# Kernel optimization log

Measured on AMD Instinct MI355X. Metric: run time of the kernel, lower is better.

Reference implementation:

```python
import jax, jax.numpy as jnp
import numpy as np

MARGIN = 1.0   # TripletLoss(margin) init arg
EPS = 1e-6     # torch F.pairwise_distance eps used by nn.TripletMarginLoss
INF = 1e9

N, D_EMB, N_CLASSES = 8192, 1024, 128


def setup_inputs() -> dict:
    key = jax.random.key(0)
    k1, k2 = jax.random.split(key)
    embeddings = jax.random.normal(k1, (N, D_EMB), dtype=jnp.float32)
    target = jax.random.randint(k2, (N,), 0, N_CLASSES, dtype=jnp.int64 if jax.config.jax_enable_x64 else jnp.int32)
    return {"embeddings": embeddings, "target": target}


def _mine_and_loss(embeddings, target):
    # Vectorized, deterministic equivalent of the per-anchor random mining loop:
    # full pairwise L2 distance matrix via a GEMM (compute-bound core).
    sq = jnp.sum(embeddings * embeddings, axis=1)                      # [N]
    d2 = sq[:, None] + sq[None, :] - 2.0 * (embeddings @ embeddings.T)  # [N, N]
    Dm = jnp.sqrt(jnp.maximum(d2, 0.0))                                 # [N, N]

    same = target[:, None] == target[None, :]
    eye = jnp.eye(target.shape[0], dtype=bool)
    pos_mask = same & ~eye          # valid positives (same class, not self)
    neg_mask = ~same                # valid negatives (different class)

    # Positive: hardest (farthest) same-class sample (deterministic stand-in
    # for the original's random positive draw).
    pos_scores = jnp.where(pos_mask, Dm, -INF)
    pos_idx = jnp.argmax(pos_scores, axis=1)                           # [N]
    d_p = jnp.max(pos_scores, axis=1)                                  # [N]

    # Negative: semi-hard (d_p < d_n < d_p + margin), pick the closest such
    # negative; if none exists, fall back to the overall hardest (min-dist)
    # negative -- mirrors the loop's early-break vs. min_dist fallback.
    semi = neg_mask & (Dm > d_p[:, None]) & (Dm < (d_p + MARGIN)[:, None])
    has_semi = jnp.any(semi, axis=1)
    neg_semi = jnp.argmin(jnp.where(semi, Dm, INF), axis=1)
    neg_hard = jnp.argmin(jnp.where(neg_mask, Dm, INF), axis=1)
    neg_idx = jnp.where(has_semi, neg_semi, neg_hard)                  # [N]

    # nn.TripletMarginLoss(margin, p=2): mean(relu(d(a,p) - d(a,n) + margin))
    # with torch's pairwise_distance eps added to the difference.
    a = embeddings
    p = embeddings[pos_idx]
    n = embeddings[neg_idx]
    dp = jnp.sqrt(jnp.sum((a - p + EPS) ** 2, axis=1))
    dn = jnp.sqrt(jnp.sum((a - n + EPS) ** 2, axis=1))
    return jnp.mean(jax.nn.relu(dp - dn + MARGIN))


def reference(embeddings, target):
    return _mine_and_loss(embeddings, target)
```

## Files before the change

### kernel.cpp

```cpp
#include <hip/hip_runtime.h>
#include <hip/hip_bf16.h>

#define N 8192
#define D 1024
#define MARGIN 1.0f
#define EPS 1e-6f

typedef __attribute__((ext_vector_type(8))) short bf16x8;
typedef __attribute__((ext_vector_type(4))) float f32x4;
typedef __attribute__((ext_vector_type(8))) _Float16 f16x8;
typedef __attribute__((ext_vector_type(4))) _Float16 f16x4;
typedef __attribute__((ext_vector_type(8))) unsigned short u16x8;

__device__ inline unsigned short f2bf(float x) {
    unsigned u = __float_as_uint(x);
    unsigned r = (u + 0x7FFFu + ((u >> 16) & 1u)) >> 16;
    return (unsigned short)r;
}

__device__ inline float h2f(unsigned hb) {
    return (float)__builtin_bit_cast(_Float16, (unsigned short)hb);
}

__global__ __launch_bounds__(256) void prep_kernel(const float* __restrict__ E,
                                                   const int* __restrict__ target,
                                                   unsigned short* __restrict__ Ebf,
                                                   float* __restrict__ sq,
                                                   unsigned char* __restrict__ cls) {
    const int r = blockIdx.x;
    const int tid = threadIdx.x;
    const float4 v = ((const float4*)(E + (size_t)r * D))[tid];
    ushort4 o;
    o.x = f2bf(v.x); o.y = f2bf(v.y); o.z = f2bf(v.z); o.w = f2bf(v.w);
    ((ushort4*)(Ebf + (size_t)r * D))[tid] = o;
    float s = v.x * v.x + v.y * v.y + v.z * v.z + v.w * v.w;
    for (int off = 32; off > 0; off >>= 1) s += __shfl_down(s, off);
    __shared__ float red[4];
    const int lane = tid & 63, wave = tid >> 6;
    if (lane == 0) red[wave] = s;
    __syncthreads();
    if (tid == 0) {
        sq[r] = red[0] + red[1] + red[2] + red[3];
        cls[r] = (unsigned char)target[r];
    }
}


#define SLOT_0A0 0
#define SLOT_0A1 16384
#define SLOT_0B0 32768
#define SLOT_0B1 49152
#define SLOT_1A0 65536
#define SLOT_1A1 81920
#define SLOT_1B0 98304
#define SLOT_1B1 114688

#define VMW(n) __asm__ __volatile__("s_waitcnt vmcnt(" #n ")" ::: "memory")
#define NOSTAGE ((void)0)
#define NOWAIT ((void)0)

#define STAGE(slotOff, baseRow, kcol) do {                                              \
    const unsigned short* _s0 = E + (size_t)((baseRow) + (tid >> 2)) * D + (kcol) + stc * 8; \
    __builtin_amdgcn_global_load_lds(                                                    \
        (const __attribute__((address_space(1))) unsigned int*)_s0,                      \
        (__attribute__((address_space(3))) unsigned int*)(smem + (slotOff) + wave * 1024), 16, 0, 0); \
    const unsigned short* _s1 = _s0 + (size_t)128 * D;                                   \
    __builtin_amdgcn_global_load_lds(                                                    \
        (const __attribute__((address_space(1))) unsigned int*)_s1,                      \
        (__attribute__((address_space(3))) unsigned int*)(smem + (slotOff) + 8192 + wave * 1024), 16, 0, 0); \
} while (0)

#define PHASE(b, ks, mq, LOADB, STG, WAIT) do {                                          \
    const char* _As = smem + (b) * 65536 + (ks) * 16384;                                 \
    const char* _Bs = smem + (b) * 65536 + 32768 + (ks) * 16384;                         \
    if (LOADB) {                                                                         \
        _Pragma("unroll") for (int nj = 0; nj < 4; ++nj)                                 \
            bfr[nj] = *(const bf16x8*)(_Bs + (wn * 64 + nj * 16 + mr) * 64 + swz);       \
    }                                                                                    \
    bf16x8 af[4];                                                                        \
    _Pragma("unroll") for (int mi = 0; mi < 4; ++mi)                                     \
        af[mi] = *(const bf16x8*)(_As + (wm * 128 + (mq) * 64 + mi * 16 + mr) * 64 + swz); \
    STG;                                                                                 \
    __builtin_amdgcn_s_setprio(1);                                                       \
    _Pragma("unroll") for (int mi = 0; mi < 4; ++mi)                                     \
        _Pragma("unroll") for (int nj = 0; nj < 4; ++nj)                                 \
            acc[(mq) * 4 + mi][nj] = __builtin_amdgcn_mfma_f32_16x16x32_bf16(            \
                af[mi], bfr[nj], acc[(mq) * 4 + mi][nj], 0, 0, 0);                       \
    __builtin_amdgcn_s_setprio(0);                                                       \
    WAIT;                                                                                \
    __asm__ __volatile__("s_barrier" ::: "memory");                                      \
} while (0)

__device__ __forceinline__ void diag_path(char* smem,
                                          const unsigned short* __restrict__ E,
                                          const float* __restrict__ sq,
                                          _Float16* __restrict__ D2h,
                                          const int c, const int tid) {
    const int lane = tid & 63;
    const int wave = tid >> 6;
    const int wmL = wave >> 2;
    const int wnL = wave & 3;
    const int mr = lane & 15;
    const int q = lane >> 4;
    const int kq = q * 8;

    const int t = c / 3, s = c - 3 * t;
    const int smi = (s + 1) >> 1;
    const int sni = s >> 1;
    const int rm = t * 256 + smi * 128;
    const int cn = t * 256 + sni * 128;
    const bool offdiag = (s == 1);

    f32x4 acc[4][2] = {};

#define DSTAGE(sl, kk) do {                                                              \
    __builtin_amdgcn_global_load_lds(                                                    \
        (const __attribute__((address_space(1))) unsigned int*)(E + (size_t)(rm + (tid >> 2)) * D + (kk) * 32 + (tid & 3) * 8), \
        (__attribute__((address_space(3))) unsigned int*)(smem + (sl) * 32768 + wave * 1024), 16, 0, 0); \
    __builtin_amdgcn_global_load_lds(                                                    \
        (const __attribute__((address_space(1))) unsigned int*)(E + (size_t)(cn + (tid >> 2)) * D + (kk) * 32 + (tid & 3) * 8), \
        (__attribute__((address_space(3))) unsigned int*)(smem + (sl) * 32768 + 16384 + wave * 1024), 16, 0, 0); \
} while (0)

#define DCOMPUTE(k) do {                                                                 \
    const unsigned short* As = (const unsigned short*)(smem + (size_t)((k) & 3) * 32768);\
    const unsigned short* Bs = As + 8192;                                                \
    bf16x8 af[4], bfv[2];                                                                \
    _Pragma("unroll") for (int mi = 0; mi < 4; ++mi)                                     \
        af[mi] = *(const bf16x8*)(As + (wmL * 64 + mi * 16 + mr) * 32 + kq);             \
    _Pragma("unroll") for (int ni = 0; ni < 2; ++ni)                                     \
        bfv[ni] = *(const bf16x8*)(Bs + (wnL * 32 + ni * 16 + mr) * 32 + kq);            \
    _Pragma("unroll") for (int mi = 0; mi < 4; ++mi)                                     \
        _Pragma("unroll") for (int ni = 0; ni < 2; ++ni)                                 \
            acc[mi][ni] = __builtin_amdgcn_mfma_f32_16x16x32_bf16(af[mi], bfv[ni], acc[mi][ni], 0, 0, 0); \
} while (0)

    DSTAGE(0, 0);
    DSTAGE(1, 1);
    for (int k = 0; k < 30; ++k) {
        DSTAGE((k + 2) & 3, k + 2);
        __asm__ __volatile__("s_waitcnt vmcnt(4)" ::: "memory");
        __asm__ __volatile__("s_barrier" ::: "memory");
        DCOMPUTE(k);
    }
    __asm__ __volatile__("s_waitcnt vmcnt(2)" ::: "memory");
    __asm__ __volatile__("s_barrier" ::: "memory");
    DCOMPUTE(30);
    __asm__ __volatile__("s_waitcnt vmcnt(0)" ::: "memory");
    __asm__ __volatile__("s_barrier" ::: "memory");
    DCOMPUTE(31);
#undef DSTAGE
#undef DCOMPUTE
    __syncthreads();

    _Float16* Ts = (_Float16*)smem;
    float sqjL[2];
#pragma unroll
    for (int ni = 0; ni < 2; ++ni) sqjL[ni] = sq[cn + wnL * 32 + ni * 16 + mr];
#pragma unroll
    for (int mi = 0; mi < 4; ++mi) {
        const int lrow = wmL * 64 + mi * 16 + q * 4;
        const int i0 = rm + lrow;
        const f32x4 sqi = *(const f32x4*)(sq + i0);
#pragma unroll
        for (int ni = 0; ni < 2; ++ni) {
            const int lcol = wnL * 32 + ni * 16 + mr;
            const int j = cn + lcol;
            f16x4 tv;
#pragma unroll
            for (int r = 0; r < 4; ++r) {
                const float d2 = fmaxf(sqi[r] + sqjL[ni] - 2.0f * acc[mi][ni][r], 0.0f);
                const _Float16 h = (_Float16)d2;
                D2h[(size_t)(i0 + r) * N + j] = h;
                tv[r] = h;
            }
            if (offdiag)
                *(f16x4*)(Ts + (size_t)lcol * 136 + lrow) = tv;
        }
    }
    if (offdiag) {
        __syncthreads();
#pragma unroll
        for (int it = 0; it < 4; ++it) {
            const int rt = it * 32 + (tid >> 4);
            const int seg = tid & 15;
            f16x8 v = *(const f16x8*)(Ts + (size_t)rt * 136 + seg * 8);
            *(f16x8*)(D2h + (size_t)(cn + rt) * N + rm + seg * 8) = v;
        }
    }
}

__global__ __launch_bounds__(512, 2) void gemm_kernel(const unsigned short* __restrict__ E,
                                                      const float* __restrict__ sq,
                                                      _Float16* __restrict__ D2h) {
    extern __shared__ char smem[];

    const int tid = threadIdx.x;

    if (blockIdx.x >= 496) {
        diag_path(smem, E, sq, D2h, blockIdx.x - 496, tid);
        return;
    }

    const int lane = tid & 63;
    const int wave = tid >> 6;
    const int wm = wave >> 2;
    const int wn = wave & 3;
    const int mr = lane & 15;
    const int q = lane >> 4;
    const int swz = ((q ^ ((mr >> 1) & 3)) << 4);
    const int stc = (tid & 3) ^ ((tid >> 3) & 3);

    const int h = blockIdx.x;
    const int l = (h & 7) * 62 + (h >> 3);

    int by = (int)((1.0f + sqrtf(8.0f * (float)l + 1.0f)) * 0.5f);
    while (by * (by - 1) / 2 > l) --by;
    while ((by + 1) * by / 2 <= l) ++by;
    const int bx = l - by * (by - 1) / 2;
    const int rm = by * 256;
    const int cn = bx * 256;

    f32x4 acc[8][4] = {};
    bf16x8 bfr[4];

    STAGE(SLOT_0A0, rm, 0);
    STAGE(SLOT_0B0, cn, 0);
    STAGE(SLOT_0A1, rm, 32);
    STAGE(SLOT_0B1, cn, 32);
    STAGE(SLOT_1A0, rm, 64);
    VMW(6);
    __asm__ __volatile__("s_barrier" ::: "memory");

    for (int i = 0; i < 7; ++i) {
        const int kt = 2 * i;
        PHASE(0, 0, 0, 1, STAGE(SLOT_1B0, cn, (kt + 1) * 64 + 0),  NOWAIT);
        PHASE(0, 0, 1, 0, STAGE(SLOT_1A1, rm, (kt + 1) * 64 + 32), VMW(6));
        PHASE(0, 1, 0, 1, STAGE(SLOT_1B1, cn, (kt + 1) * 64 + 32), NOWAIT);
        PHASE(0, 1, 1, 0, STAGE(SLOT_0A0, rm, (kt + 2) * 64 + 0),  VMW(6));
        PHASE(1, 0, 0, 1, STAGE(SLOT_0B0, cn, (kt + 2) * 64 + 0),  NOWAIT);
        PHASE(1, 0, 1, 0, STAGE(SLOT_0A1, rm, (kt + 2) * 64 + 32), VMW(6));
        PHASE(1, 1, 0, 1, STAGE(SLOT_0B1, cn, (kt + 2) * 64 + 32), NOWAIT);
        PHASE(1, 1, 1, 0, STAGE(SLOT_1A0, rm, (kt + 3) * 64 + 0),  VMW(6));
    }
    PHASE(0, 0, 0, 1, STAGE(SLOT_1B0, cn, 15 * 64 + 0),  NOWAIT);
    PHASE(0, 0, 1, 0, STAGE(SLOT_1A1, rm, 15 * 64 + 32), VMW(6));
    PHASE(0, 1, 0, 1, STAGE(SLOT_1B1, cn, 15 * 64 + 32), NOWAIT);
    PHASE(0, 1, 1, 0, NOSTAGE, VMW(4));
    PHASE(1, 0, 0, 1, NOSTAGE, NOWAIT);
    PHASE(1, 0, 1, 0, NOSTAGE, VMW(0));
    PHASE(1, 1, 0, 1, NOSTAGE, NOWAIT);
    PHASE(1, 1, 1, 0, NOSTAGE, NOWAIT);

    __asm__ __volatile__("s_waitcnt lgkmcnt(0)" ::: "memory");
    __asm__ __volatile__("s_barrier" ::: "memory");

    const int crow = q * 4;
    float sqj[4];
#pragma unroll
    for (int nj = 0; nj < 4; ++nj) sqj[nj] = sq[cn + wn * 64 + nj * 16 + mr];
    float sqiv[8][4];
#pragma unroll
    for (int mg = 0; mg < 8; ++mg) {
        const f32x4 s4 = *(const f32x4*)(sq + rm + wm * 128 + mg * 16 + crow);
#pragma unroll
        for (int r = 0; r < 4; ++r) sqiv[mg][r] = s4[r];
    }

#pragma unroll
    for (int mg = 0; mg < 8; ++mg) {
        const int ilocb = wm * 128 + mg * 16 + crow;
#pragma unroll
        for (int nj = 0; nj < 4; ++nj) {
            const int jloc = wn * 64 + nj * 16 + mr;
            const unsigned jc = (unsigned)jloc >> 3;
            const unsigned jo = ((unsigned)jloc & 7) << 1;
#pragma unroll
            for (int r = 0; r < 4; ++r) {
                const float d2 = fmaxf(sqiv[mg][r] + sqj[nj] - 2.0f * acc[mg][nj][r], 0.0f);
                const int row = ilocb + r;
                *(_Float16*)(smem + (size_t)row * 512 + ((jc ^ (row & 31)) << 4) + jo) = (_Float16)d2;
            }
        }
    }
    __asm__ __volatile__("s_waitcnt lgkmcnt(0)" ::: "memory");
    __asm__ __volatile__("s_barrier" ::: "memory");
    {
        const int seg = tid & 31;
#pragma unroll
        for (int it = 0; it < 16; ++it) {
            const int rt = it * 16 + (tid >> 5);
            f16x8 v = *(const f16x8*)(smem + (size_t)rt * 512 + (((unsigned)seg ^ (rt & 31)) << 4));
            *(f16x8*)(D2h + (size_t)(rm + rt) * N + cn + seg * 8) = v;
        }
    }
    __asm__ __volatile__("s_waitcnt lgkmcnt(0)" ::: "memory");
    __asm__ __volatile__("s_barrier" ::: "memory");

#pragma unroll
    for (int mg = 0; mg < 8; ++mg) {
        const int iloc = wm * 128 + mg * 16 + crow;
        const unsigned cch = (unsigned)iloc >> 3;
        const unsigned cof = ((unsigned)iloc & 7) << 1;
#pragma unroll
        for (int nj = 0; nj < 4; ++nj) {
            const int jloc = wn * 64 + nj * 16 + mr;
            f16x4 tv;
#pragma unroll
            for (int r = 0; r < 4; ++r)
                tv[r] = (_Float16)fmaxf(sqiv[mg][r] + sqj[nj] - 2.0f * acc[mg][nj][r], 0.0f);
            *(f16x4*)(smem + (size_t)jloc * 512 + ((cch ^ (jloc & 31)) << 4) + cof) = tv;
        }
    }
    __asm__ __volatile__("s_waitcnt lgkmcnt(0)" ::: "memory");
    __asm__ __volatile__("s_barrier" ::: "memory");
    {
        const int seg = tid & 31;
#pragma unroll
        for (int it = 0; it < 16; ++it) {
            const int rt = it * 16 + (tid >> 5);
            f16x8 v = *(const f16x8*)(smem + (size_t)rt * 512 + (((unsigned)seg ^ (rt & 31)) << 4));
            *(f16x8*)(D2h + (size_t)(cn + rt) * N + rm + seg * 8) = v;
        }
    }
}

__global__ __launch_bounds__(256) void mine_kernel(const _Float16* __restrict__ D2h,
                                                   const unsigned char* __restrict__ cls,
                                                   float* __restrict__ loss_arr) {
    const int i = blockIdx.x;
    const int tid = threadIdx.x;
    const int lane = tid & 63, wave = tid >> 6;
    const unsigned tcb = cls[i];
    const unsigned short* row = (const unsigned short*)(D2h + (size_t)i * N);

    u16x8 v[4];
    unsigned long long c8[4];
#pragma unroll
    for (int it = 0; it < 4; ++it) {
        v[it] = *(const u16x8*)(row + it * 2048 + tid * 8);
        c8[it] = *(const unsigned long long*)(cls + it * 2048 + tid * 8);
    }

    unsigned pm = 0u, nm = 0xFFFFu;
#pragma unroll
    for (int it = 0; it < 4; ++it) {
#pragma unroll
        for (int e = 0; e < 8; ++e) {
            const unsigned hb = v[it][e];
            const bool s = ((unsigned)(c8[it] >> (8 * e)) & 0xFFu) == tcb;
            pm = max(pm, s ? hb : 0u);
            nm = min(nm, s ? 0xFFFFu : hb);
        }
    }
    for (int off = 1; off < 64; off <<= 1) {
        pm = max(pm, (unsigned)__shfl_xor((int)pm, off));
        nm = min(nm, (unsigned)__shfl_xor((int)nm, off));
    }
    __shared__ unsigned redp[4], redn[4], reds[4];
    if (lane == 0) { redp[wave] = pm; redn[wave] = nm; }
    __syncthreads();
    pm = max(max(redp[0], redp[1]), max(redp[2], redp[3]));
    nm = min(min(redn[0], redn[1]), min(redn[2], redn[3]));
    const unsigned lob = pm;

    unsigned sm = 0xFFFFu;
#pragma unroll
    for (int it = 0; it < 4; ++it) {
#pragma unroll
        for (int e = 0; e < 8; ++e) {
            const unsigned hb = v[it][e];
            sm = min(sm, hb > lob ? hb : 0xFFFFu);
        }
    }
    for (int off = 1; off < 64; off <<= 1)
        sm = min(sm, (unsigned)__shfl_xor((int)sm, off));
    if (lane == 0) reds[wave] = sm;
    __syncthreads();
    if (tid == 0) {
        sm = min(min(reds[0], reds[1]), min(reds[2], reds[3]));
        const float lo = h2f(lob);
        const float dp = sqrtf(lo);
        const float hw = dp + MARGIN;
        const float hi = hw * hw;
        const float smv = h2f(sm);
        const float dn2 = (smv < hi) ? smv : h2f(nm);
        loss_arr[i] = fmaxf(dp - sqrtf(dn2) + MARGIN, 0.0f);
    }
}

__global__ __launch_bounds__(256) void reduce_kernel(const float* __restrict__ loss_arr,
                                                     float* __restrict__ out) {
    const int tid = threadIdx.x;
    float s = 0.0f;
    for (int k = tid; k < N; k += 256) s += loss_arr[k];
    for (int off = 32; off > 0; off >>= 1) s += __shfl_down(s, off);
    __shared__ float red[4];
    const int lane = tid & 63, wave = tid >> 6;
    if (lane == 0) red[wave] = s;
    __syncthreads();
    if (tid == 0) out[0] = (red[0] + red[1] + red[2] + red[3]) * (1.0f / N);
}

extern "C" void kernel_launch(void* const* d_in, const int* in_sizes, int n_in,
                              void* d_out, int out_size, void* d_ws, size_t ws_size,
                              hipStream_t stream) {
    const float* E = (const float*)d_in[0];
    const int* target = (const int*)d_in[1];
    float* out = (float*)d_out;
    char* ws = (char*)d_ws;

    unsigned short* Ebf = (unsigned short*)ws;
    float* sq        = (float*)(ws + (size_t)16777216);
    float* loss_arr  = (float*)(ws + (size_t)16809984);
    unsigned char* cls = (unsigned char*)(ws + (size_t)16842752);
    _Float16* D2h    = (_Float16*)(ws + (size_t)16875520);

    static bool attr_set = false;
    if (!attr_set) {
        hipFuncSetAttribute((const void*)gemm_kernel,
                            hipFuncAttributeMaxDynamicSharedMemorySize, 131072);
        attr_set = true;
    }

    prep_kernel<<<N, 256, 0, stream>>>(E, target, Ebf, sq, cls);
    gemm_kernel<<<592, 512, 131072, stream>>>(Ebf, sq, D2h);
    mine_kernel<<<N, 256, 0, stream>>>(D2h, cls, loss_arr);
    reduce_kernel<<<1, 256, 0, stream>>>(loss_arr, out);
}
```

Before: 192.7 us.

## Batch rows per block in prep and mine kernels; reorder GEMM tile mapping

The prep kernel now handles four rows per block, one wave per row, which drops the shared-memory reduction and barrier. The mine kernel processes two distance rows per block so the class-label loads are shared between them and the launch count is halved. The GEMM triangular tile index mapping is replaced with a grouped scheme that walks 4-row strips, changing which tiles run concurrently and so their L2 reuse. The risks are more register pressure in the mine kernel and a new tile mapping that must still cover every lower-triangular tile exactly once.

New measurement: 185.8 us. -3.6%, faster.

```diff
diff --git a/kernel.cpp b/kernel.cpp
--- a/kernel.cpp
+++ b/kernel.cpp
@@ -27,20 +27,17 @@
                                                    unsigned short* __restrict__ Ebf,
                                                    float* __restrict__ sq,
                                                    unsigned char* __restrict__ cls) {
-    const int r = blockIdx.x;
     const int tid = threadIdx.x;
-    const float4 v = ((const float4*)(E + (size_t)r * D))[tid];
+    const int lane = tid & 63, wave = tid >> 6;
+    const int r = blockIdx.x * 4 + wave;
+    const float4 v = ((const float4*)(E + (size_t)r * D))[lane];
     ushort4 o;
     o.x = f2bf(v.x); o.y = f2bf(v.y); o.z = f2bf(v.z); o.w = f2bf(v.w);
-    ((ushort4*)(Ebf + (size_t)r * D))[tid] = o;
+    ((ushort4*)(Ebf + (size_t)r * D))[lane] = o;
     float s = v.x * v.x + v.y * v.y + v.z * v.z + v.w * v.w;
     for (int off = 32; off > 0; off >>= 1) s += __shfl_down(s, off);
-    __shared__ float red[4];
-    const int lane = tid & 63, wave = tid >> 6;
-    if (lane == 0) red[wave] = s;
-    __syncthreads();
-    if (tid == 0) {
-        sq[r] = red[0] + red[1] + red[2] + red[3];
+    if (lane == 0) {
+        sq[r] = s;
         cls[r] = (unsigned char)target[r];
     }
 }
@@ -214,10 +211,20 @@
     const int h = blockIdx.x;
     const int l = (h & 7) * 62 + (h >> 3);
 
-    int by = (int)((1.0f + sqrtf(8.0f * (float)l + 1.0f)) * 0.5f);
-    while (by * (by - 1) / 2 > l) --by;
-    while ((by + 1) * by / 2 <= l) ++by;
-    const int bx = l - by * (by - 1) / 2;
+    int s = (int)((2.0f + sqrtf(4.0f + 32.0f * (float)l)) * 0.0625f);
+    while (8 * (s + 1) * (s + 1) - 2 * (s + 1) <= l) ++s;
+    while (8 * s * s - 2 * s > l) --s;
+    const int o = l - (8 * s * s - 2 * s);
+    int by, bx;
+    if (o < 16 * s) {
+        bx = o >> 2;
+        by = 4 * s + (o & 3);
+    } else {
+        const int o2 = o - 16 * s;
+        if (o2 < 3)      { bx = 4 * s;     by = 4 * s + 1 + o2; }
+        else if (o2 < 5) { bx = 4 * s + 1; by = 4 * s + 2 + (o2 - 3); }
+        else             { bx = 4 * s + 2; by = 4 * s + 3; }
+    }
     const int rm = by * 256;
     const int cn = bx * 256;
 
@@ -328,64 +335,88 @@
 __global__ __launch_bounds__(256) void mine_kernel(const _Float16* __restrict__ D2h,
                                                    const unsigned char* __restrict__ cls,
                                                    float* __restrict__ loss_arr) {
-    const int i = blockIdx.x;
+    const int i0 = blockIdx.x * 2;
     const int tid = threadIdx.x;
     const int lane = tid & 63, wave = tid >> 6;
-    const unsigned tcb = cls[i];
-    const unsigned short* row = (const unsigned short*)(D2h + (size_t)i * N);
-
-    u16x8 v[4];
+    const unsigned tcbA = cls[i0];
+    const unsigned tcbB = cls[i0 + 1];
+    const unsigned short* rowA = (const unsigned short*)(D2h + (size_t)i0 * N);
+    const unsigned short* rowB = rowA + N;
+
+    u16x8 va[4], vb[4];
     unsigned long long c8[4];
 #pragma unroll
     for (int it = 0; it < 4; ++it) {
-        v[it] = *(const u16x8*)(row + it * 2048 + tid * 8);
+        va[it] = *(const u16x8*)(rowA + it * 2048 + tid * 8);
+        vb[it] = *(const u16x8*)(rowB + it * 2048 + tid * 8);
         c8[it] = *(const unsigned long long*)(cls + it * 2048 + tid * 8);
     }
 
-    unsigned pm = 0u, nm = 0xFFFFu;
+    unsigned pmA = 0u, nmA = 0xFFFFu, pmB = 0u, nmB = 0xFFFFu;
 #pragma unroll
     for (int it = 0; it < 4; ++it) {
 #pragma unroll
         for (int e = 0; e < 8; ++e) {
-            const unsigned hb = v[it][e];
-            const bool s = ((unsigned)(c8[it] >> (8 * e)) & 0xFFu) == tcb;
-            pm = max(pm, s ? hb : 0u);
-            nm = min(nm, s ? 0xFFFFu : hb);
+            const unsigned cv = (unsigned)(c8[it] >> (8 * e)) & 0xFFu;
+            const unsigned ha = va[it][e];
+            const unsigned hb = vb[it][e];
+            const bool sA = (cv == tcbA);
+            const bool sB = (cv == tcbB);
+            pmA = max(pmA, sA ? ha : 0u);
+            nmA = min(nmA, sA ? 0xFFFFu : ha);
+            pmB = max(pmB, sB ? hb : 0u);
+            nmB = min(nmB, sB ? 0xFFFFu : hb);
         }
     }
     for (int off = 1; off < 64; off <<= 1) {
-        pm = max(pm, (unsigned)__shfl_xor((int)pm, off));
-        nm = min(nm, (unsigned)__shfl_xor((int)nm, off));
-    }
-    __shared__ unsigned redp[4], redn[4], reds[4];
-    if (lane == 0) { redp[wave] = pm; redn[wave] = nm; }
+        pmA = max(pmA, (unsigned)__shfl_xor((int)pmA, off));
+        nmA = min(nmA, (unsigned)__shfl_xor((int)nmA, off));
+        pmB = max(pmB, (unsigned)__shfl_xor((int)pmB, off));
+        nmB = min(nmB, (unsigned)__shfl_xor((int)nmB, off));
+    }
+    __shared__ unsigned redp[2][4], redn[2][4], reds[2][4];
+    if (lane == 0) {
+        redp[0][wave] = pmA; redn[0][wave] = nmA;
+        redp[1][wave] = pmB; redn[1][wave] = nmB;
+    }
     __syncthreads();
-    pm = max(max(redp[0], redp[1]), max(redp[2], redp[3]));
-    nm = min(min(redn[0], redn[1]), min(redn[2], redn[3]));
-    const unsigned lob = pm;
-
-    unsigned sm = 0xFFFFu;
+    pmA = max(max(redp[0][0], redp[0][1]), max(redp[0][2], redp[0][3]));
+    nmA = min(min(redn[0][0], redn[0][1]), min(redn[0][2], redn[0][3]));
+    pmB = max(max(redp[1][0], redp[1][1]), max(redp[1][2], redp[1][3]));
+    nmB = min(min(redn[1][0], redn[1][1]), min(redn[1][2], redn[1][3]));
+
+    unsigned smA = 0xFFFFu, smB = 0xFFFFu;
 #pragma unroll
     for (int it = 0; it < 4; ++it) {
 #pragma unroll
         for (int e = 0; e < 8; ++e) {
-            const unsigned hb = v[it][e];
-            sm = min(sm, hb > lob ? hb : 0xFFFFu);
-        }
-    }
-    for (int off = 1; off < 64; off <<= 1)
-        sm = min(sm, (unsigned)__shfl_xor((int)sm, off));
-    if (lane == 0) reds[wave] = sm;
+            const unsigned ha = va[it][e];
+            const unsigned hb = vb[it][e];
+            smA = min(smA, ha > pmA ? ha : 0xFFFFu);
+            smB = min(smB, hb > pmB ? hb : 0xFFFFu);
+        }
+    }
+    for (int off = 1; off < 64; off <<= 1) {
+        smA = min(smA, (unsigned)__shfl_xor((int)smA, off));
+        smB = min(smB, (unsigned)__shfl_xor((int)smB, off));
+    }
+    if (lane == 0) { reds[0][wave] = smA; reds[1][wave] = smB; }
     __syncthreads();
     if (tid == 0) {
-        sm = min(min(reds[0], reds[1]), min(reds[2], reds[3]));
-        const float lo = h2f(lob);
-        const float dp = sqrtf(lo);
-        const float hw = dp + MARGIN;
-        const float hi = hw * hw;
-        const float smv = h2f(sm);
-        const float dn2 = (smv < hi) ? smv : h2f(nm);
-        loss_arr[i] = fmaxf(dp - sqrtf(dn2) + MARGIN, 0.0f);
+#pragma unroll
+        for (int rr = 0; rr < 2; ++rr) {
+            const unsigned lob = rr ? pmB : pmA;
+            const unsigned nm = rr ? nmB : nmA;
+            const unsigned sm = min(min(reds[rr][0], reds[rr][1]),
+                                    min(reds[rr][2], reds[rr][3]));
+            const float lo = h2f(lob);
+            const float dp = sqrtf(lo);
+            const float hw = dp + MARGIN;
+            const float hi = hw * hw;
+            const float smv = h2f(sm);
+            const float dn2 = (smv < hi) ? smv : h2f(nm);
+            loss_arr[i0 + rr] = fmaxf(dp - sqrtf(dn2) + MARGIN, 0.0f);
+        }
     }
 }
 
@@ -423,8 +454,8 @@
         attr_set = true;
     }
 
-    prep_kernel<<<N, 256, 0, stream>>>(E, target, Ebf, sq, cls);
+    prep_kernel<<<N / 4, 256, 0, stream>>>(E, target, Ebf, sq, cls);
     gemm_kernel<<<592, 512, 131072, stream>>>(Ebf, sq, D2h);
-    mine_kernel<<<N, 256, 0, stream>>>(D2h, cls, loss_arr);
+    mine_kernel<<<N / 2, 256, 0, stream>>>(D2h, cls, loss_arr);
     reduce_kernel<<<1, 256, 0, stream>>>(loss_arr, out);
 }
```

## Fuse positive/hardest-negative mining into GEMM epilogue, drop symmetric transpose write

Applied to the files above, without the earlier changes.

The GEMM epilogue now computes per-row and per-column hardest-positive and hardest-negative values directly from the accumulators. It reduces them through shared-memory atomics and then global atomicMax/atomicMin. Because the symmetric tile is covered by column reductions, the transposed half of the fp16 distance matrix is no longer written. The old full-row mine kernel is replaced by a tile-wise semi-hard pass over the upper triangle only, plus a small finalize kernel. This halves the distance-matrix traffic, at the cost of many atomics and an extra launch. The prep kernel is also repacked to one row per wave and now initialises the reduction buffers.

Measured after the change: 204.5 us. +6.2%, slower.

```diff
diff --git a/kernel.cpp b/kernel.cpp
--- a/kernel.cpp
+++ b/kernel.cpp
@@ -22,26 +22,33 @@
     return (float)__builtin_bit_cast(_Float16, (unsigned short)hb);
 }
 
+__device__ inline unsigned h2u(float d2) {
+    return (unsigned)__builtin_bit_cast(unsigned short, (_Float16)d2);
+}
+
 __global__ __launch_bounds__(256) void prep_kernel(const float* __restrict__ E,
                                                    const int* __restrict__ target,
                                                    unsigned short* __restrict__ Ebf,
                                                    float* __restrict__ sq,
-                                                   unsigned char* __restrict__ cls) {
-    const int r = blockIdx.x;
+                                                   unsigned char* __restrict__ cls,
+                                                   unsigned* __restrict__ pmG,
+                                                   unsigned* __restrict__ nmG,
+                                                   unsigned* __restrict__ smG) {
     const int tid = threadIdx.x;
-    const float4 v = ((const float4*)(E + (size_t)r * D))[tid];
+    const int lane = tid & 63, wave = tid >> 6;
+    const int r = blockIdx.x * 4 + wave;
+    const float4 v = ((const float4*)(E + (size_t)r * D))[lane];
     ushort4 o;
     o.x = f2bf(v.x); o.y = f2bf(v.y); o.z = f2bf(v.z); o.w = f2bf(v.w);
-    ((ushort4*)(Ebf + (size_t)r * D))[tid] = o;
+    ((ushort4*)(Ebf + (size_t)r * D))[lane] = o;
     float s = v.x * v.x + v.y * v.y + v.z * v.z + v.w * v.w;
     for (int off = 32; off > 0; off >>= 1) s += __shfl_down(s, off);
-    __shared__ float red[4];
-    const int lane = tid & 63, wave = tid >> 6;
-    if (lane == 0) red[wave] = s;
-    __syncthreads();
-    if (tid == 0) {
-        sq[r] = red[0] + red[1] + red[2] + red[3];
+    if (lane == 0) {
+        sq[r] = s;
         cls[r] = (unsigned char)target[r];
+        pmG[r] = 0u;
+        nmG[r] = 0xFFFFFFFFu;
+        smG[r] = 0xFFFFFFFFu;
     }
 }
 
@@ -94,7 +101,10 @@
 __device__ __forceinline__ void diag_path(char* smem,
                                           const unsigned short* __restrict__ E,
                                           const float* __restrict__ sq,
+                                          const unsigned char* __restrict__ cls,
                                           _Float16* __restrict__ D2h,
+                                          unsigned* __restrict__ pmG,
+                                          unsigned* __restrict__ nmG,
                                           const int c, const int tid) {
     const int lane = tid & 63;
     const int wave = tid >> 6;
@@ -109,7 +119,6 @@
     const int sni = s >> 1;
     const int rm = t * 256 + smi * 128;
     const int cn = t * 256 + sni * 128;
-    const bool offdiag = (s == 1);
 
     f32x4 acc[4][2] = {};
 
@@ -153,52 +162,108 @@
 #undef DCOMPUTE
     __syncthreads();
 
-    _Float16* Ts = (_Float16*)smem;
+    unsigned ccbL[2];
     float sqjL[2];
 #pragma unroll
-    for (int ni = 0; ni < 2; ++ni) sqjL[ni] = sq[cn + wnL * 32 + ni * 16 + mr];
+    for (int ni = 0; ni < 2; ++ni) {
+        const int col = cn + wnL * 32 + ni * 16 + mr;
+        sqjL[ni] = sq[col];
+        ccbL[ni] = cls[col];
+    }
+
 #pragma unroll
     for (int mi = 0; mi < 4; ++mi) {
-        const int lrow = wmL * 64 + mi * 16 + q * 4;
-        const int i0 = rm + lrow;
+        const int i0 = rm + wmL * 64 + mi * 16 + q * 4;
         const f32x4 sqi = *(const f32x4*)(sq + i0);
 #pragma unroll
         for (int ni = 0; ni < 2; ++ni) {
-            const int lcol = wnL * 32 + ni * 16 + mr;
-            const int j = cn + lcol;
-            f16x4 tv;
+            const int j = cn + wnL * 32 + ni * 16 + mr;
 #pragma unroll
             for (int r = 0; r < 4; ++r) {
                 const float d2 = fmaxf(sqi[r] + sqjL[ni] - 2.0f * acc[mi][ni][r], 0.0f);
-                const _Float16 h = (_Float16)d2;
-                D2h[(size_t)(i0 + r) * N + j] = h;
-                tv[r] = h;
-            }
-            if (offdiag)
-                *(f16x4*)(Ts + (size_t)lcol * 136 + lrow) = tv;
-        }
-    }
-    if (offdiag) {
-        __syncthreads();
-#pragma unroll
-        for (int it = 0; it < 4; ++it) {
-            const int rt = it * 32 + (tid >> 4);
-            const int seg = tid & 15;
-            f16x8 v = *(const f16x8*)(Ts + (size_t)rt * 136 + seg * 8);
-            *(f16x8*)(D2h + (size_t)(cn + rt) * N + rm + seg * 8) = v;
-        }
+                D2h[(size_t)(i0 + r) * N + j] = (_Float16)d2;
+            }
+        }
+    }
+
+    unsigned* pmRowL = (unsigned*)smem;
+    unsigned* nmRowL = pmRowL + 128;
+    unsigned* pmColL = pmRowL + 256;
+    unsigned* nmColL = pmRowL + 384;
+    if (tid < 128)       pmRowL[tid] = 0u;
+    else if (tid < 256)  nmRowL[tid - 128] = 0xFFFFFFFFu;
+    else if (tid < 384)  pmColL[tid - 256] = 0u;
+    else                 nmColL[tid - 384] = 0xFFFFFFFFu;
+    __syncthreads();
+
+    unsigned cpm[2] = {0u, 0u}, cnm[2] = {0xFFFFu, 0xFFFFu};
+#pragma unroll
+    for (int mi = 0; mi < 4; ++mi) {
+        const int i0 = rm + wmL * 64 + mi * 16 + q * 4;
+        const unsigned clsR = *(const unsigned*)(cls + i0);
+        const f32x4 sqi = *(const f32x4*)(sq + i0);
+        unsigned rpm[4] = {0u, 0u, 0u, 0u};
+        unsigned rnm[4] = {0xFFFFu, 0xFFFFu, 0xFFFFu, 0xFFFFu};
+#pragma unroll
+        for (int ni = 0; ni < 2; ++ni) {
+#pragma unroll
+            for (int r = 0; r < 4; ++r) {
+                const unsigned v = h2u(fmaxf(sqi[r] + sqjL[ni] - 2.0f * acc[mi][ni][r], 0.0f));
+                const bool same = ((clsR >> (8 * r)) & 0xFFu) == ccbL[ni];
+                rpm[r] = max(rpm[r], same ? v : 0u);
+                rnm[r] = min(rnm[r], same ? 0xFFFFu : v);
+                cpm[ni] = max(cpm[ni], same ? v : 0u);
+                cnm[ni] = min(cnm[ni], same ? 0xFFFFu : v);
+            }
+        }
+#pragma unroll
+        for (int r = 0; r < 4; ++r) {
+            for (int off = 1; off < 16; off <<= 1) {
+                rpm[r] = max(rpm[r], (unsigned)__shfl_xor((int)rpm[r], off));
+                rnm[r] = min(rnm[r], (unsigned)__shfl_xor((int)rnm[r], off));
+            }
+            if (mr == 0) {
+                const int li = wmL * 64 + mi * 16 + q * 4 + r;
+                atomicMax(&pmRowL[li], rpm[r]);
+                atomicMin(&nmRowL[li], rnm[r]);
+            }
+        }
+    }
+#pragma unroll
+    for (int ni = 0; ni < 2; ++ni) {
+        cpm[ni] = max(cpm[ni], (unsigned)__shfl_xor((int)cpm[ni], 16));
+        cpm[ni] = max(cpm[ni], (unsigned)__shfl_xor((int)cpm[ni], 32));
+        cnm[ni] = min(cnm[ni], (unsigned)__shfl_xor((int)cnm[ni], 16));
+        cnm[ni] = min(cnm[ni], (unsigned)__shfl_xor((int)cnm[ni], 32));
+        if (q == 0) {
+            const int lj = wnL * 32 + ni * 16 + mr;
+            atomicMax(&pmColL[lj], cpm[ni]);
+            atomicMin(&nmColL[lj], cnm[ni]);
+        }
+    }
+    __syncthreads();
+    if (tid < 128) {
+        atomicMax(&pmG[rm + tid], pmRowL[tid]);
+        atomicMin(&nmG[rm + tid], nmRowL[tid]);
+    } else if (tid < 256) {
+        const int c2 = tid - 128;
+        atomicMax(&pmG[cn + c2], pmColL[c2]);
+        atomicMin(&nmG[cn + c2], nmColL[c2]);
     }
 }
 
 __global__ __launch_bounds__(512, 2) void gemm_kernel(const unsigned short* __restrict__ E,
                                                       const float* __restrict__ sq,
-                                                      _Float16* __restrict__ D2h) {
+                                                      const unsigned char* __restrict__ cls,
+                                                      _Float16* __restrict__ D2h,
+                                                      unsigned* __restrict__ pmG,
+                                                      unsigned* __restrict__ nmG) {
     extern __shared__ char smem[];
 
     const int tid = threadIdx.x;
 
     if (blockIdx.x >= 496) {
-        diag_path(smem, E, sq, D2h, blockIdx.x - 496, tid);
+        diag_path(smem, E, sq, cls, D2h, pmG, nmG, blockIdx.x - 496, tid);
         return;
     }
 
@@ -213,7 +278,6 @@
 
     const int h = blockIdx.x;
     const int l = (h & 7) * 62 + (h >> 3);
-
     int by = (int)((1.0f + sqrtf(8.0f * (float)l + 1.0f)) * 0.5f);
     while (by * (by - 1) / 2 > l) --by;
     while ((by + 1) * by / 2 <= l) ++by;
@@ -257,8 +321,13 @@
 
     const int crow = q * 4;
     float sqj[4];
-#pragma unroll
-    for (int nj = 0; nj < 4; ++nj) sqj[nj] = sq[cn + wn * 64 + nj * 16 + mr];
+    unsigned ccb[4];
+#pragma unroll
+    for (int nj = 0; nj < 4; ++nj) {
+        const int col = cn + wn * 64 + nj * 16 + mr;
+        sqj[nj] = sq[col];
+        ccb[nj] = cls[col];
+    }
     float sqiv[8][4];
 #pragma unroll
     for (int mg = 0; mg < 8; ++mg) {
@@ -297,96 +366,185 @@
     __asm__ __volatile__("s_waitcnt lgkmcnt(0)" ::: "memory");
     __asm__ __volatile__("s_barrier" ::: "memory");
 
+    unsigned* pmRow = (unsigned*)smem;
+    unsigned* nmRow = pmRow + 256;
+    unsigned* pmCol = pmRow + 512;
+    unsigned* nmCol = pmRow + 768;
+    if (tid < 256) { pmRow[tid] = 0u; nmRow[tid] = 0xFFFFFFFFu; }
+    else           { pmCol[tid - 256] = 0u; nmCol[tid - 256] = 0xFFFFFFFFu; }
+    __syncthreads();
+
+    unsigned cpm[4] = {0u, 0u, 0u, 0u};
+    unsigned cnm[4] = {0xFFFFu, 0xFFFFu, 0xFFFFu, 0xFFFFu};
 #pragma unroll
     for (int mg = 0; mg < 8; ++mg) {
-        const int iloc = wm * 128 + mg * 16 + crow;
-        const unsigned cch = (unsigned)iloc >> 3;
-        const unsigned cof = ((unsigned)iloc & 7) << 1;
+        const unsigned clsR = *(const unsigned*)(cls + rm + wm * 128 + mg * 16 + crow);
+        unsigned rpm[4] = {0u, 0u, 0u, 0u};
+        unsigned rnm[4] = {0xFFFFu, 0xFFFFu, 0xFFFFu, 0xFFFFu};
 #pragma unroll
         for (int nj = 0; nj < 4; ++nj) {
-            const int jloc = wn * 64 + nj * 16 + mr;
-            f16x4 tv;
-#pragma unroll
-            for (int r = 0; r < 4; ++r)
-                tv[r] = (_Float16)fmaxf(sqiv[mg][r] + sqj[nj] - 2.0f * acc[mg][nj][r], 0.0f);
-            *(f16x4*)(smem + (size_t)jloc * 512 + ((cch ^ (jloc & 31)) << 4) + cof) = tv;
-        }
-    }
-    __asm__ __volatile__("s_waitcnt lgkmcnt(0)" ::: "memory");
-    __asm__ __volatile__("s_barrier" ::: "memory");
-    {
-        const int seg = tid & 31;
-#pragma unroll
-        for (int it = 0; it < 16; ++it) {
-            const int rt = it * 16 + (tid >> 5);
-            f16x8 v = *(const f16x8*)(smem + (size_t)rt * 512 + (((unsigned)seg ^ (rt & 31)) << 4));
-            *(f16x8*)(D2h + (size_t)(cn + rt) * N + rm + seg * 8) = v;
-        }
-    }
-}
-
-__global__ __launch_bounds__(256) void mine_kernel(const _Float16* __restrict__ D2h,
-                                                   const unsigned char* __restrict__ cls,
-                                                   float* __restrict__ loss_arr) {
-    const int i = blockIdx.x;
+#pragma unroll
+            for (int r = 0; r < 4; ++r) {
+                const unsigned v = h2u(fmaxf(sqiv[mg][r] + sqj[nj] - 2.0f * acc[mg][nj][r], 0.0f));
+                const bool same = ((clsR >> (8 * r)) & 0xFFu) == ccb[nj];
+                rpm[r] = max(rpm[r], same ? v : 0u);
+                rnm[r] = min(rnm[r], same ? 0xFFFFu : v);
+                cpm[nj] = max(cpm[nj], same ? v : 0u);
+                cnm[nj] = min(cnm[nj], same ? 0xFFFFu : v);
+            }
+        }
+#pragma unroll
+        for (int r = 0; r < 4; ++r) {
+            for (int off = 1; off < 16; off <<= 1) {
+                rpm[r] = max(rpm[r], (unsigned)__shfl_xor((int)rpm[r], off));
+                rnm[r] = min(rnm[r], (unsigned)__shfl_xor((int)rnm[r], off));
+            }
+            if (mr == 0) {
+                const int li = wm * 128 + mg * 16 + crow + r;
+                atomicMax(&pmRow[li], rpm[r]);
+                atomicMin(&nmRow[li], rnm[r]);
+            }
+        }
+    }
+#pragma unroll
+    for (int nj = 0; nj < 4; ++nj) {
+        cpm[nj] = max(cpm[nj], (unsigned)__shfl_xor((int)cpm[nj], 16));
+        cpm[nj] = max(cpm[nj], (unsigned)__shfl_xor((int)cpm[nj], 32));
+        cnm[nj] = min(cnm[nj], (unsigned)__shfl_xor((int)cnm[nj], 16));
+        cnm[nj] = min(cnm[nj], (unsigned)__shfl_xor((int)cnm[nj], 32));
+        if (q == 0) {
+            const int lj = wn * 64 + nj * 16 + mr;
+            atomicMax(&pmCol[lj], cpm[nj]);
+            atomicMin(&nmCol[lj], cnm[nj]);
+        }
+    }
+    __syncthreads();
+    if (tid < 256) {
+        atomicMax(&pmG[rm + tid], pmRow[tid]);
+        atomicMin(&nmG[rm + tid], nmRow[tid]);
+    } else {
+        const int c2 = tid - 256;
+        atomicMax(&pmG[cn + c2], pmCol[c2]);
+        atomicMin(&nmG[cn + c2], nmCol[c2]);
+    }
+}
+
+__global__ __launch_bounds__(512) void mine2_kernel(const _Float16* __restrict__ D2h,
+                                                    const unsigned* __restrict__ pmG,
+                                                    unsigned* __restrict__ smG) {
+    __shared__ unsigned colMin[256];
     const int tid = threadIdx.x;
-    const int lane = tid & 63, wave = tid >> 6;
-    const unsigned tcb = cls[i];
-    const unsigned short* row = (const unsigned short*)(D2h + (size_t)i * N);
-
-    u16x8 v[4];
-    unsigned long long c8[4];
-#pragma unroll
-    for (int it = 0; it < 4; ++it) {
-        v[it] = *(const u16x8*)(row + it * 2048 + tid * 8);
-        c8[it] = *(const unsigned long long*)(cls + it * 2048 + tid * 8);
-    }
-
-    unsigned pm = 0u, nm = 0xFFFFu;
-#pragma unroll
-    for (int it = 0; it < 4; ++it) {
-#pragma unroll
-        for (int e = 0; e < 8; ++e) {
-            const unsigned hb = v[it][e];
-            const bool s = ((unsigned)(c8[it] >> (8 * e)) & 0xFFu) == tcb;
-            pm = max(pm, s ? hb : 0u);
-            nm = min(nm, s ? 0xFFFFu : hb);
-        }
-    }
-    for (int off = 1; off < 64; off <<= 1) {
-        pm = max(pm, (unsigned)__shfl_xor((int)pm, off));
-        nm = min(nm, (unsigned)__shfl_xor((int)nm, off));
-    }
-    __shared__ unsigned redp[4], redn[4], reds[4];
-    if (lane == 0) { redp[wave] = pm; redn[wave] = nm; }
-    __syncthreads();
-    pm = max(max(redp[0], redp[1]), max(redp[2], redp[3]));
-    nm = min(min(redn[0], redn[1]), min(redn[2], redn[3]));
-    const unsigned lob = pm;
-
-    unsigned sm = 0xFFFFu;
-#pragma unroll
-    for (int it = 0; it < 4; ++it) {
-#pragma unroll
-        for (int e = 0; e < 8; ++e) {
-            const unsigned hb = v[it][e];
-            sm = min(sm, hb > lob ? hb : 0xFFFFu);
-        }
-    }
-    for (int off = 1; off < 64; off <<= 1)
-        sm = min(sm, (unsigned)__shfl_xor((int)sm, off));
-    if (lane == 0) reds[wave] = sm;
-    __syncthreads();
-    if (tid == 0) {
-        sm = min(min(reds[0], reds[1]), min(reds[2], reds[3]));
-        const float lo = h2f(lob);
-        const float dp = sqrtf(lo);
-        const float hw = dp + MARGIN;
-        const float hi = hw * hw;
-        const float smv = h2f(sm);
-        const float dn2 = (smv < hi) ? smv : h2f(nm);
-        loss_arr[i] = fmaxf(dp - sqrtf(dn2) + MARGIN, 0.0f);
-    }
+    const int lane = tid & 63;
+
+    if (blockIdx.x < 496) {
+        const int l = blockIdx.x;
+        int by = (int)((1.0f + sqrtf(8.0f * (float)l + 1.0f)) * 0.5f);
+        while (by * (by - 1) / 2 > l) --by;
+        while ((by + 1) * by / 2 <= l) ++by;
+        const int bx = l - by * (by - 1) / 2;
+        const int rm = by * 256;
+        const int cn = bx * 256;
+
+        const int tr = tid >> 4;
+        const int tc = tid & 15;
+        unsigned pmc[16], cmin[16];
+#pragma unroll
+        for (int k = 0; k < 16; ++k) { pmc[k] = pmG[cn + tc * 16 + k]; cmin[k] = 0xFFFFu; }
+#pragma unroll
+        for (int ri = 0; ri < 8; ++ri) {
+            const int r = tr + 32 * ri;
+            const unsigned short* rp = (const unsigned short*)(D2h + (size_t)(rm + r) * N + cn + tc * 16);
+            const u16x8 a = *(const u16x8*)rp;
+            const u16x8 b = *(const u16x8*)(rp + 8);
+            const unsigned pmr = pmG[rm + r];
+            unsigned rmin = 0xFFFFu;
+#pragma unroll
+            for (int k = 0; k < 8; ++k) {
+                const unsigned v = a[k];
+                rmin = min(rmin, v > pmr ? v : 0xFFFFu);
+                cmin[k] = min(cmin[k], v > pmc[k] ? v : 0xFFFFu);
+                const unsigned w = b[k];
+                rmin = min(rmin, w > pmr ? w : 0xFFFFu);
+                cmin[k + 8] = min(cmin[k + 8], w > pmc[k + 8] ? w : 0xFFFFu);
+            }
+            for (int off = 1; off < 16; off <<= 1)
+                rmin = min(rmin, (unsigned)__shfl_xor((int)rmin, off));
+            if (tc == 0) atomicMin(&smG[rm + r], rmin);
+        }
+#pragma unroll
+        for (int k = 0; k < 16; ++k) {
+            cmin[k] = min(cmin[k], (unsigned)__shfl_xor((int)cmin[k], 16));
+            cmin[k] = min(cmin[k], (unsigned)__shfl_xor((int)cmin[k], 32));
+        }
+        if (tid < 256) colMin[tid] = 0xFFFFu;
+        __syncthreads();
+        if (lane < 16) {
+#pragma unroll
+            for (int k = 0; k < 16; ++k) atomicMin(&colMin[tc * 16 + k], cmin[k]);
+        }
+        __syncthreads();
+        if (tid < 256) atomicMin(&smG[cn + tid], colMin[tid]);
+    } else {
+        const int c = blockIdx.x - 496;
+        const int t = c / 3, s = c - 3 * t;
+        const int rm = t * 256 + (((s + 1) >> 1) << 7);
+        const int cn = t * 256 + ((s >> 1) << 7);
+
+        const int tr = tid >> 3;
+        const int tc = tid & 7;
+        unsigned pmc[16], cmin[16];
+#pragma unroll
+        for (int k = 0; k < 16; ++k) { pmc[k] = pmG[cn + tc * 16 + k]; cmin[k] = 0xFFFFu; }
+#pragma unroll
+        for (int ri = 0; ri < 2; ++ri) {
+            const int r = tr + 64 * ri;
+            const unsigned short* rp = (const unsigned short*)(D2h + (size_t)(rm + r) * N + cn + tc * 16);
+            const u16x8 a = *(const u16x8*)rp;
+            const u16x8 b = *(const u16x8*)(rp + 8);
+            const unsigned pmr = pmG[rm + r];
+            unsigned rmin = 0xFFFFu;
+#pragma unroll
+            for (int k = 0; k < 8; ++k) {
+                const unsigned v = a[k];
+                rmin = min(rmin, v > pmr ? v : 0xFFFFu);
+                cmin[k] = min(cmin[k], v > pmc[k] ? v : 0xFFFFu);
+                const unsigned w = b[k];
+                rmin = min(rmin, w > pmr ? w : 0xFFFFu);
+                cmin[k + 8] = min(cmin[k + 8], w > pmc[k + 8] ? w : 0xFFFFu);
+            }
+            for (int off = 1; off < 8; off <<= 1)
+                rmin = min(rmin, (unsigned)__shfl_xor((int)rmin, off));
+            if (tc == 0) atomicMin(&smG[rm + r], rmin);
+        }
+#pragma unroll
+        for (int k = 0; k < 16; ++k) {
+            cmin[k] = min(cmin[k], (unsigned)__shfl_xor((int)cmin[k], 8));
+            cmin[k] = min(cmin[k], (unsigned)__shfl_xor((int)cmin[k], 16));
+            cmin[k] = min(cmin[k], (unsigned)__shfl_xor((int)cmin[k], 32));
+        }
+        if (tid < 128) colMin[tid] = 0xFFFFu;
+        __syncthreads();
+        if (lane < 8) {
+#pragma unroll
+            for (int k = 0; k < 16; ++k) atomicMin(&colMin[tc * 16 + k], cmin[k]);
+        }
+        __syncthreads();
+        if (tid < 128) atomicMin(&smG[cn + tid], colMin[tid]);
+    }
+}
+
+__global__ __launch_bounds__(256) void finalize_kernel(const unsigned* __restrict__ pmG,
+                                                       const unsigned* __restrict__ nmG,
+                                                       const unsigned* __restrict__ smG,
+                                                       float* __restrict__ loss_arr) {
+    const int i = blockIdx.x * 256 + threadIdx.x;
+    const float lo = h2f(pmG[i] & 0xFFFFu);
+    const float dp = sqrtf(lo);
+    const float hw = dp + MARGIN;
+    const float hi = hw * hw;
+    const float smv = h2f(smG[i] & 0xFFFFu);
+    const float dn2 = (smv < hi) ? smv : h2f(nmG[i] & 0xFFFFu);
+    loss_arr[i] = fmaxf(dp - sqrtf(dn2) + MARGIN, 0.0f);
 }
 
 __global__ __launch_bounds__(256) void reduce_kernel(const float* __restrict__ loss_arr,
@@ -415,6 +573,9 @@
     float* loss_arr  = (float*)(ws + (size_t)16809984);
     unsigned char* cls = (unsigned char*)(ws + (size_t)16842752);
     _Float16* D2h    = (_Float16*)(ws + (size_t)16875520);
+    unsigned* pmG    = (unsigned*)(ws + (size_t)151093248);
+    unsigned* nmG    = (unsigned*)(ws + (size_t)151126016);
+    unsigned* smG    = (unsigned*)(ws + (size_t)151158784);
 
     static bool attr_set = false;
     if (!attr_set) {
@@ -423,8 +584,9 @@
         attr_set = true;
     }
 
-    prep_kernel<<<N, 256, 0, stream>>>(E, target, Ebf, sq, cls);
-    gemm_kernel<<<592, 512, 131072, stream>>>(Ebf, sq, D2h);
-    mine_kernel<<<N, 256, 0, stream>>>(D2h, cls, loss_arr);
+    prep_kernel<<<N / 4, 256, 0, stream>>>(E, target, Ebf, sq, cls, pmG, nmG, smG);
+    gemm_kernel<<<592, 512, 131072, stream>>>(Ebf, sq, cls, D2h, pmG, nmG);
+    mine2_kernel<<<592, 512, 0, stream>>>(D2h, pmG, smG);
+    finalize_kernel<<<N / 256, 256, 0, stream>>>(pmG, nmG, smG, loss_arr);
     reduce_kernel<<<1, 256, 0, stream>>>(loss_arr, out);
 }
```
